# Kernel tuning notes

Hardware: AMD Instinct MI355X
Metric: run time of the kernel (lower is better)

## Reference

```python
import math
import jax, jax.numpy as jnp
import numpy as np

D = 512; H = 8; DH = 64          # d_model, heads, head dim
AB = 8                            # attention block size (BigBird block)
NG, NW, NR = 2, 5, 3              # global / window / random blocks
K = NG + NW + NR                  # attended blocks per query block
NL = 5                            # layers per (encoder|decoder) stack
MAXSEQ = 1024; BS = 4; NM = 4; LAT = 16; FF = 2048


def setup_inputs() -> dict:
    key = jax.random.key(0)
    ks = jax.random.split(key, 20)
    B = 32
    S_enc = MAXSEQ + 1
    nb_enc = (S_enc + AB - 1) // AB   # 129
    nb_dec = MAXSEQ // AB             # 128
    def n(i, shape, s=0.02):
        return jax.random.normal(ks[i], shape, jnp.float32) * s
    return {
        'x': jax.random.normal(ks[0], (B, MAXSEQ, BS * NM), jnp.float32),
        'eps': jax.random.normal(ks[1], (B, LAT), jnp.float32),
        'emb_in': n(2, (S_enc, D)),
        'emb_out': n(3, (MAXSEQ, D)),
        'W_data': n(4, (BS * NM, D)), 'b_data': jnp.zeros((D,), jnp.float32),
        'Wqkv': n(5, (2 * NL, D, 3 * D)), 'bqkv': jnp.zeros((2 * NL, 3 * D), jnp.float32),
        'Wo': n(6, (2 * NL, D, D)), 'bo': jnp.zeros((2 * NL, D), jnp.float32),
        'ln1_g': jnp.ones((2 * NL, D), jnp.float32), 'ln1_b': jnp.zeros((2 * NL, D), jnp.float32),
        'W1': n(7, (2 * NL, D, FF)), 'b1': jnp.zeros((2 * NL, FF), jnp.float32),
        'W2': n(8, (2 * NL, FF, D)), 'b2': jnp.zeros((2 * NL, D), jnp.float32),
        'ln2_g': jnp.ones((2 * NL, D), jnp.float32), 'ln2_b': jnp.zeros((2 * NL, D), jnp.float32),
        'W_mean': n(9, (D, LAT)), 'b_mean': jnp.zeros((LAT,), jnp.float32),
        'W_lv': n(10, (D, LAT)), 'b_lv': jnp.zeros((LAT,), jnp.float32),
        'W_exp': n(11, (LAT, 2 * MAXSEQ)), 'b_exp': jnp.zeros((2 * MAXSEQ,), jnp.float32),
        'W_conv': n(12, (2, D)), 'b_conv': jnp.zeros((D,), jnp.float32),
        'W_seq': n(13, (D, BS * NM)), 'b_seq': jnp.zeros((BS * NM,), jnp.float32),
        'rand_enc': jax.random.randint(ks[14], (nb_enc, NR), 0, nb_enc, jnp.int32),
        'rand_dec': jax.random.randint(ks[15], (nb_dec, NR), 0, nb_dec, jnp.int32),
    }


def _ln(x, g, b):
    m = jnp.mean(x, -1, keepdims=True)
    v = jnp.var(x, -1, keepdims=True)
    return (x - m) * jax.lax.rsqrt(v + 1e-5) * g + b


def _block_index(nb, rand):
    # per query block: NG global blocks, NW window blocks, NR random blocks
    i = jnp.arange(nb)
    g = jnp.broadcast_to(jnp.arange(NG)[None, :], (nb, NG))
    w = i[:, None] + (jnp.arange(NW) - NW // 2)[None, :]
    w_valid = (w >= 0) & (w < nb)
    idx = jnp.concatenate([g, jnp.clip(w, 0, nb - 1), rand], axis=1)          # [nb, K]
    valid = jnp.concatenate([jnp.ones((nb, NG), bool), w_valid,
                             jnp.ones((nb, NR), bool)], axis=1)               # [nb, K]
    return idx, valid


def _sparse_attn(x, Wqkv, bqkv, Wo, bo, rand):
    # BigBird-style block-sparse self attention (global + window + random blocks)
    B, S, _ = x.shape
    nb = (S + AB - 1) // AB
    Sp = nb * AB
    qkv = jnp.pad(x @ Wqkv + bqkv, ((0, 0), (0, Sp - S), (0, 0)))
    q, k, v = jnp.split(qkv, 3, axis=-1)
    def blk(t):  # [B,Sp,D] -> [B,H,nb,AB,DH]
        return t.reshape(B, nb, AB, H, DH).transpose(0, 3, 1, 2, 4)
    q, k, v = blk(q), blk(k), blk(v)
    idx, bvalid = _block_index(nb, rand)
    kg = k[:, :, idx]                      # [B,H,nb,K,AB,DH]
    vg = v[:, :, idx]
    scores = jnp.einsum('bhnqd,bhnkpd->bhnqkp', q, kg) / math.sqrt(DH)  # [B,H,nb,AB,K,AB]
    tok_valid = (jnp.arange(Sp) < S).reshape(nb, AB)
    kmask = bvalid[:, :, None] & tok_valid[idx]                          # [nb,K,AB]
    scores = jnp.where(kmask[None, None, :, None], scores, -1e9)
    attn = jax.nn.softmax(scores.reshape(B, H, nb, AB, K * AB), axis=-1)
    out = jnp.einsum('bhnqk,bhnkd->bhnqd', attn, vg.reshape(B, H, nb, K * AB, DH))
    out = out.transpose(0, 2, 3, 1, 4).reshape(B, Sp, D)[:, :S]
    return out @ Wo + bo


def _layer(x, i, p, rand):
    (Wqkv, bqkv, Wo, bo, ln1_g, ln1_b, W1, b1, W2, b2, ln2_g, ln2_b) = p
    a = _sparse_attn(x, Wqkv[i], bqkv[i], Wo[i], bo[i], rand)
    x = _ln(x + a, ln1_g[i], ln1_b[i])
    f = jax.nn.relu(x @ W1[i] + b1[i]) @ W2[i] + b2[i]
    return _ln(x + f, ln2_g[i], ln2_b[i])


def _forward(x, eps, emb_in, emb_out, W_data, b_data, Wqkv, bqkv, Wo, bo,
             ln1_g, ln1_b, W1, b1, W2, b2, ln2_g, ln2_b, W_mean, b_mean,
             W_lv, b_lv, W_exp, b_exp, W_conv, b_conv, W_seq, b_seq,
             rand_enc, rand_dec):
    B = x.shape[0]
    p = (Wqkv, bqkv, Wo, bo, ln1_g, ln1_b, W1, b1, W2, b2, ln2_g, ln2_b)
    # ---- encode ----
    h = x @ W_data + b_data                                   # [B,1024,512]
    cls = jnp.zeros((B, 1, D), x.dtype)
    h = jnp.concatenate([cls, h], axis=1) + emb_in            # [B,1025,512]
    for i in range(NL):
        h = _layer(h, i, p, rand_enc)
    pooled = h[:, 0]
    mean = pooled @ W_mean + b_mean
    logvar = pooled @ W_lv + b_lv
    # ---- sample (diag-Gaussian rsample) ----
    z = mean + eps * jnp.exp(0.5 * logvar)
    # ---- decode ----
    seq = (z @ W_exp + b_exp).reshape(B, 2, MAXSEQ)           # [B,2,1024]
    d = jnp.einsum('bcs,cd->bsd', seq, W_conv) + b_conv       # 1x1 conv, -> [B,1024,512]
    d = d + emb_out
    for i in range(NL, 2 * NL):
        d = _layer(d, i, p, rand_dec)
    out = d @ W_seq + b_seq                                   # [B,1024,16] (1x1 conv)
    decoded = out.reshape(B, -1, NM)                          # [B,4096,4]
    elbo = jnp.mean(-0.5 * jnp.sum(1.0 + logvar - mean ** 2 - jnp.exp(logvar), axis=1))
    return decoded, elbo


def reference(x, eps, emb_in, emb_out, W_data, b_data, Wqkv, bqkv, Wo, bo,
              ln1_g, ln1_b, W1, b1, W2, b2, ln2_g, ln2_b, W_mean, b_mean,
              W_lv, b_lv, W_exp, b_exp, W_conv, b_conv, W_seq, b_seq,
              rand_enc, rand_dec):
    return _forward(x, eps, emb_in, emb_out, W_data, b_data, Wqkv, bqkv, Wo, bo,
                    ln1_g, ln1_b, W1, b1, W2, b2, ln2_g, ln2_b, W_mean, b_mean,
                    W_lv, b_lv, W_exp, b_exp, W_conv, b_conv, W_seq, b_seq,
                    rand_enc, rand_dec)
```

## Files before the change

### kernel.cpp

```cpp
#include <hip/hip_runtime.h>

typedef unsigned short u16;
typedef __attribute__((ext_vector_type(8))) short short8;
typedef __attribute__((ext_vector_type(4))) float f32x4;

__device__ __forceinline__ float b2f(u16 h) {
  union { unsigned int u; float f; } v; v.u = ((unsigned int)h) << 16; return v.f;
}
__device__ __forceinline__ u16 f2b(float f) {
  union { float f; unsigned int u; } v; v.f = f;
  return (u16)((v.u + 0x7fffu + ((v.u >> 16) & 1u)) >> 16);
}

__device__ __forceinline__ void gload16(const u16* g, u16* l) {
  __builtin_amdgcn_global_load_lds(
      (const __attribute__((address_space(1))) void*)g,
      (__attribute__((address_space(3))) void*)l, 16, 0, 0);
}

#define SENC 1025
#define SPENC 1032
#define NBE 129
#define SDEC 1024
#define NBD 128
#define BATCH 32
#define MENC (BATCH * SPENC)
#define MDEC (BATCH * SDEC)

__global__ void beacon_k(float* out) { if (threadIdx.x == 0) out[0] = 1000.0f; }

__global__ __launch_bounds__(256) void tr_k(const float* __restrict__ W, u16* __restrict__ WT, int K, int N)
{
  __shared__ float sm[32][33];
  int k0 = blockIdx.x * 32, n0 = blockIdx.y * 32;
  const float* Wz = W + (size_t)blockIdx.z * K * N;
  u16* WTz = WT + (size_t)blockIdx.z * K * N;
  int r = threadIdx.x >> 3, c0 = (threadIdx.x & 7) * 4;
  float4 v = *(const float4*)&Wz[(size_t)(k0 + r) * N + n0 + c0];
  sm[r][c0] = v.x; sm[r][c0 + 1] = v.y; sm[r][c0 + 2] = v.z; sm[r][c0 + 3] = v.w;
  __syncthreads();
  ushort4 u;
  u.x = f2b(sm[c0][r]); u.y = f2b(sm[c0 + 1][r]); u.z = f2b(sm[c0 + 2][r]); u.w = f2b(sm[c0 + 3][r]);
  *(ushort4*)&WTz[(size_t)(n0 + r) * K + k0 + c0] = u;
}

__global__ __launch_bounds__(256) void embed_k(const float* __restrict__ x, const float* __restrict__ Wd,
    const float* __restrict__ bd, const float* __restrict__ emb, float* __restrict__ h, u16* __restrict__ hb)
{
  size_t gid = (size_t)blockIdx.x * 256 + threadIdx.x;
  int dd = (int)(gid & 511);
  size_t rs = gid >> 9;
  int s = (int)(rs % SPENC);
  int b = (int)(rs / SPENC);
  float v;
  if (s == 0) {
    v = emb[dd];
  } else if (s < SENC) {
    float acc = bd[dd];
    const float* xr = x + ((size_t)b * 1024 + (s - 1)) * 16;
    #pragma unroll
    for (int j = 0; j < 16; ++j) acc += xr[j] * Wd[j * 512 + dd];
    v = acc + emb[(size_t)s * 512 + dd];
  } else {
    v = 0.f;
  }
  h[gid] = v;
  hb[gid] = f2b(v);
}

template<bool RELU>
__global__ __launch_bounds__(512) void mgemm_k(const u16* __restrict__ A, const u16* __restrict__ WT,
    const float* __restrict__ bias, u16* __restrict__ C,
    int M, int N, int Kc, int lda, int ldb)
{
  __shared__ __align__(16) u16 sA[3][128 * 32];
  __shared__ __align__(16) u16 sB[3][256 * 32];
  int t = threadIdx.x;

  int gx = gridDim.x;
  int nwg = gx * gridDim.y;
  int flat = blockIdx.y * gx + blockIdx.x;
  int q = nwg >> 3, rr = nwg & 7;
  int xcd = flat & 7, idx = flat >> 3;
  int swz = (xcd < rr ? xcd * (q + 1) : rr * (q + 1) + (xcd - rr) * q) + idx;
  int bx = swz % gx, by = swz / gx;

  int n0 = bx * 256, m0 = by * 128;
  int lane = t & 63, wave = t >> 6;
  int wm = (wave >> 2) * 64, wn = (wave & 3) * 64;
  int quad = lane >> 4, l15 = lane & 15;

  int rA = t >> 2, sc = t & 3;
  int cA = sc ^ ((rA >> 1) & 3);
  int raA = m0 + rA; raA = raA < M ? raA : M - 1;
  const u16* gA  = A  + (size_t)raA * lda + cA * 8;
  const u16* gB0 = WT + (size_t)(n0 + rA) * ldb + cA * 8;
  const u16* gB1 = WT + (size_t)(n0 + 128 + rA) * ldb + cA * 8;

  f32x4 acc[4][4];
  #pragma unroll
  for (int i = 0; i < 4; ++i)
    #pragma unroll
    for (int j = 0; j < 4; ++j) acc[i][j] = (f32x4){0.f, 0.f, 0.f, 0.f};

  const int nt = Kc >> 5;
  gload16(gA,      &sA[0][t * 8]);
  gload16(gB0,     &sB[0][t * 8]);
  gload16(gB1,     &sB[0][(512 + t) * 8]);
  gload16(gA + 32, &sA[1][t * 8]);
  gload16(gB0 + 32,&sB[1][t * 8]);
  gload16(gB1 + 32,&sB[1][(512 + t) * 8]);

  int cur = 0;
  for (int tt = 0; tt < nt; ++tt) {
    if (tt < nt - 1) {
      asm volatile("s_waitcnt vmcnt(3)" ::: "memory");
    } else {
      asm volatile("s_waitcnt vmcnt(0)" ::: "memory");
    }
    __builtin_amdgcn_s_barrier();
    asm volatile("" ::: "memory");
    if (tt + 2 < nt) {
      int k0 = (tt + 2) << 5;
      int nb = tt + 2; nb -= (nb / 3) * 3;
      gload16(gA + k0,  &sA[nb][t * 8]);
      gload16(gB0 + k0, &sB[nb][t * 8]);
      gload16(gB1 + k0, &sB[nb][(512 + t) * 8]);
    }
    short8 af[4], bf[4];
    #pragma unroll
    for (int i = 0; i < 4; ++i) {
      int ra = wm + i * 16 + l15;
      af[i] = *(const short8*)&sA[cur][ra * 32 + (quad ^ ((ra >> 1) & 3)) * 8];
    }
    #pragma unroll
    for (int j = 0; j < 4; ++j) {
      int rb = wn + j * 16 + l15;
      bf[j] = *(const short8*)&sB[cur][rb * 32 + (quad ^ ((rb >> 1) & 3)) * 8];
    }
    __builtin_amdgcn_s_setprio(1);
    #pragma unroll
    for (int i = 0; i < 4; ++i)
      #pragma unroll
      for (int j = 0; j < 4; ++j)
        acc[i][j] = __builtin_amdgcn_mfma_f32_16x16x32_bf16(af[i], bf[j], acc[i][j], 0, 0, 0);
    __builtin_amdgcn_s_setprio(0);
    cur = (cur == 2) ? 0 : cur + 1;
  }

  #pragma unroll
  for (int i = 0; i < 4; ++i) {
    int mBase = m0 + wm + i * 16 + quad * 4;
    #pragma unroll
    for (int r = 0; r < 4; ++r) {
      int m = mBase + r;
      if (m < M) {
        #pragma unroll
        for (int j = 0; j < 4; ++j) {
          int n = n0 + wn + j * 16 + l15;
          float v = acc[i][j][r] + bias[n];
          if (RELU) v = fmaxf(v, 0.f);
          C[(size_t)m * N + n] = f2b(v);
        }
      }
    }
  }
}

__global__ __launch_bounds__(512) void mgemmln_k(const u16* __restrict__ A, const u16* __restrict__ WT,
    const float* __restrict__ bias, float* __restrict__ h, u16* __restrict__ hb,
    const float* __restrict__ g, const float* __restrict__ bbv_,
    int M, int Kc, int lda)
{
  __shared__ __align__(16) u16 sA[2][128 * 32];
  __shared__ __align__(16) u16 sB[2][512 * 32];
  __shared__ float redS[128][4], redQ[128][4];
  int t = threadIdx.x;
  int m0 = blockIdx.x * 128;
  int lane = t & 63, wave = t >> 6;
  int wm = (wave >> 2) * 64, wn = (wave & 3) * 128;
  int quad = lane >> 4, l15 = lane & 15;
  int wnid = wave & 3;

  int rA = t >> 2, sc = t & 3;
  int cA = sc ^ ((rA >> 1) & 3);
  const u16* gA = A + (size_t)(m0 + rA) * lda + cA * 8;
  const u16* gB = WT + (size_t)rA * Kc + cA * 8;

  f32x4 acc[4][8];
  #pragma unroll
  for (int i = 0; i < 4; ++i)
    #pragma unroll
    for (int j = 0; j < 8; ++j) acc[i][j] = (f32x4){0.f, 0.f, 0.f, 0.f};

  const int nt = Kc >> 5;
  gload16(gA, &sA[0][t * 8]);
  #pragma unroll
  for (int b4 = 0; b4 < 4; ++b4)
    gload16(gB + (size_t)b4 * 128 * Kc, &sB[0][(b4 * 512 + t) * 8]);
  int cur = 0;
  for (int tt = 0; tt < nt; ++tt) {
    __syncthreads();
    if (tt + 1 < nt) {
      int k0 = (tt + 1) << 5;
      gload16(gA + k0, &sA[cur ^ 1][t * 8]);
      #pragma unroll
      for (int b4 = 0; b4 < 4; ++b4)
        gload16(gB + (size_t)b4 * 128 * Kc + k0, &sB[cur ^ 1][(b4 * 512 + t) * 8]);
    }
    short8 af[4], bf[8];
    #pragma unroll
    for (int i = 0; i < 4; ++i) {
      int ra = wm + i * 16 + l15;
      af[i] = *(const short8*)&sA[cur][ra * 32 + (quad ^ ((ra >> 1) & 3)) * 8];
    }
    #pragma unroll
    for (int j = 0; j < 8; ++j) {
      int rb = wn + j * 16 + l15;
      bf[j] = *(const short8*)&sB[cur][rb * 32 + (quad ^ ((rb >> 1) & 3)) * 8];
    }
    __builtin_amdgcn_s_setprio(1);
    #pragma unroll
    for (int i = 0; i < 4; ++i)
      #pragma unroll
      for (int j = 0; j < 8; ++j)
        acc[i][j] = __builtin_amdgcn_mfma_f32_16x16x32_bf16(af[i], bf[j], acc[i][j], 0, 0, 0);
    __builtin_amdgcn_s_setprio(0);
    cur ^= 1;
  }

  float bsv[8];
  #pragma unroll
  for (int j = 0; j < 8; ++j) bsv[j] = bias[wn + j * 16 + l15];

  #pragma unroll
  for (int i = 0; i < 4; ++i) {
    #pragma unroll
    for (int r = 0; r < 4; ++r) {
      int lr = wm + i * 16 + quad * 4 + r;
      const float* hrow = h + (size_t)(m0 + lr) * 512 + wn + l15;
      float s = 0.f, qq = 0.f;
      #pragma unroll
      for (int j = 0; j < 8; ++j) {
        float v = acc[i][j][r] + bsv[j] + hrow[j * 16];
        acc[i][j][r] = v;
        s += v; qq += v * v;
      }
      #pragma unroll
      for (int off = 1; off < 16; off <<= 1) {
        s += __shfl_xor(s, off);
        qq += __shfl_xor(qq, off);
      }
      if (l15 == 0) { redS[lr][wnid] = s; redQ[lr][wnid] = qq; }
    }
  }
  __syncthreads();
  float gv[8], bv[8];
  #pragma unroll
  for (int j = 0; j < 8; ++j) {
    gv[j] = g[wn + j * 16 + l15];
    bv[j] = bbv_[wn + j * 16 + l15];
  }
  #pragma unroll
  for (int i = 0; i < 4; ++i) {
    #pragma unroll
    for (int r = 0; r < 4; ++r) {
      int lr = wm + i * 16 + quad * 4 + r;
      float s = redS[lr][0] + redS[lr][1] + redS[lr][2] + redS[lr][3];
      float qq = redQ[lr][0] + redQ[lr][1] + redQ[lr][2] + redQ[lr][3];
      float mean = s * (1.f / 512.f);
      float var = fmaxf(qq * (1.f / 512.f) - mean * mean, 0.f);
      float rinv = rsqrtf(var + 1e-5f);
      float* hrow = h + (size_t)(m0 + lr) * 512 + wn + l15;
      u16* hbrow = hb + (size_t)(m0 + lr) * 512 + wn + l15;
      #pragma unroll
      for (int j = 0; j < 8; ++j) {
        float o = (acc[i][j][r] - mean) * rinv * gv[j] + bv[j];
        hrow[j * 16] = o;
        hbrow[j * 16] = f2b(o);
      }
    }
  }
}

__global__ __launch_bounds__(64) void attnm_k(const u16* __restrict__ qkv, u16* __restrict__ av,
    const int* __restrict__ rnd, int S, int Sp, int nb)
{
  __shared__ __align__(16) u16 Vt[64 * 104];
  __shared__ __align__(16) u16 Pl[16 * 104];
  __shared__ int sJB[10], sVD[10];
  int t = threadIdx.x;
  int n = blockIdx.x % nb;
  int r1 = blockIdx.x / nb;
  int hh = r1 & 7, b = r1 >> 3;
  const u16* base = qkv + (size_t)b * Sp * 1536;
  int l15 = t & 15, quad = t >> 4;

  if (t < 10) {
    int jb, vd;
    if (t < 2) { jb = t; vd = 1; }
    else if (t < 7) {
      int w = n + t - 4;
      vd = (w >= 0 && w < nb) ? 1 : 0;
      jb = w < 0 ? 0 : (w > nb - 1 ? nb - 1 : w);
    } else { jb = rnd[n * 3 + t - 7]; vd = 1; }
    sJB[t] = jb; sVD[t] = vd;
  }
  {
    f32x4 zz = {0.f, 0.f, 0.f, 0.f};
    *(f32x4*)&Vt[t * 104 + 80] = zz;
    *(f32x4*)&Vt[t * 104 + 88] = zz;
    if (t < 16) {
      *(f32x4*)&Pl[t * 104 + 80] = zz;
      *(f32x4*)&Pl[t * 104 + 88] = zz;
    }
  }
  __syncthreads();

  short8 aq0, aq1;
  {
    const u16* qp = base + (size_t)(n * 8 + (l15 & 7)) * 1536 + hh * 64 + quad * 8;
    aq0 = *(const short8*)qp;
    aq1 = *(const short8*)(qp + 32);
  }

  f32x4 s[5];
  float okm[5];
  #pragma unroll
  for (int tile = 0; tile < 5; ++tile) {
    int kb = tile * 2 + (l15 >> 3);
    int tok = sJB[kb] * 8 + (l15 & 7);
    okm[tile] = (sVD[kb] && tok < S) ? 0.f : -3.0e38f;
    const u16* kp = base + (size_t)tok * 1536 + 512 + hh * 64 + quad * 8;
    short8 k0 = *(const short8*)kp;
    short8 k1 = *(const short8*)(kp + 32);
    f32x4 c = {0.f, 0.f, 0.f, 0.f};
    c = __builtin_amdgcn_mfma_f32_16x16x32_bf16(aq0, k0, c, 0, 0, 0);
    c = __builtin_amdgcn_mfma_f32_16x16x32_bf16(aq1, k1, c, 0, 0, 0);
    s[tile] = c;
  }

  u16 vreg[80];
  #pragma unroll
  for (int vt = 0; vt < 10; ++vt) {
    const u16* vp = base + (size_t)(sJB[vt] * 8) * 1536 + 1024 + hh * 64 + t;
    #pragma unroll
    for (int j = 0; j < 8; ++j) vreg[vt * 8 + j] = vp[(size_t)j * 1536];
  }

  f32x4 mx = {-3.0e38f, -3.0e38f, -3.0e38f, -3.0e38f};
  #pragma unroll
  for (int tile = 0; tile < 5; ++tile) {
    #pragma unroll
    for (int r = 0; r < 4; ++r) {
      float v = s[tile][r] * 0.125f + okm[tile];
      s[tile][r] = v;
      mx[r] = fmaxf(mx[r], v);
    }
  }
  #pragma unroll
  for (int off = 1; off < 16; off <<= 1) {
    #pragma unroll
    for (int r = 0; r < 4; ++r) mx[r] = fmaxf(mx[r], __shfl_xor(mx[r], off));
  }
  f32x4 sm = {0.f, 0.f, 0.f, 0.f};
  #pragma unroll
  for (int tile = 0; tile < 5; ++tile) {
    #pragma unroll
    for (int r = 0; r < 4; ++r) {
      float e = __expf(s[tile][r] - mx[r]);
      s[tile][r] = e;
      sm[r] += e;
    }
  }
  #pragma unroll
  for (int off = 1; off < 16; off <<= 1) {
    #pragma unroll
    for (int r = 0; r < 4; ++r) sm[r] += __shfl_xor(sm[r], off);
  }

  #pragma unroll
  for (int tile = 0; tile < 5; ++tile)
    #pragma unroll
    for (int r = 0; r < 4; ++r)
      Pl[(quad * 4 + r) * 104 + tile * 16 + l15] = f2b(s[tile][r]);

  #pragma unroll
  for (int vt = 0; vt < 10; ++vt) {
    short8 w;
    #pragma unroll
    for (int j = 0; j < 8; ++j) ((u16*)&w)[j] = (short)vreg[vt * 8 + j];
    *(short8*)&Vt[t * 104 + vt * 8] = w;
  }
  __syncthreads();

  f32x4 o[4];
  #pragma unroll
  for (int dn = 0; dn < 4; ++dn) o[dn] = (f32x4){0.f, 0.f, 0.f, 0.f};
  #pragma unroll
  for (int ks = 0; ks < 3; ++ks) {
    short8 ap = *(const short8*)&Pl[l15 * 104 + ks * 32 + quad * 8];
    #pragma unroll
    for (int dn = 0; dn < 4; ++dn) {
      short8 bv = *(const short8*)&Vt[(dn * 16 + l15) * 104 + ks * 32 + quad * 8];
      o[dn] = __builtin_amdgcn_mfma_f32_16x16x32_bf16(ap, bv, o[dn], 0, 0, 0);
    }
  }

  if (quad < 2) {
    #pragma unroll
    for (int r = 0; r < 4; ++r) {
      int qi = quad * 4 + r;
      float inv = 1.f / sm[r];
      u16* op = av + ((size_t)b * Sp + n * 8 + qi) * 512 + hh * 64 + l15;
      #pragma unroll
      for (int dn = 0; dn < 4; ++dn)
        op[dn * 16] = f2b(o[dn][r] * inv);
    }
  }
}

__global__ __launch_bounds__(512) void head_k(const float* __restrict__ h,
    const float* __restrict__ Wm, const float* __restrict__ bm,
    const float* __restrict__ Wlv, const float* __restrict__ blv,
    const float* __restrict__ eps, float* __restrict__ z, float* out_elbo)
{
  __shared__ float red[512];
  int t = threadIdx.x;
  int b = t >> 4, i = t & 15;
  const float* p = h + (size_t)b * SPENC * 512;
  float am = bm[i], al = blv[i];
  for (int c = 0; c < 512; ++c) {
    float pv = p[c];
    am += pv * Wm[c * 16 + i];
    al += pv * Wlv[c * 16 + i];
  }
  z[t] = am + eps[t] * expf(0.5f * al);
  red[t] = -0.5f * (1.f + al - am * am - expf(al));
  __syncthreads();
  for (int o = 256; o > 0; o >>= 1) { if (t < o) red[t] += red[t + o]; __syncthreads(); }
  if (t == 0) out_elbo[0] = red[0] * (1.f / 32.f);
}

__global__ __launch_bounds__(256) void seq_k(const float* __restrict__ z, const float* __restrict__ We,
    const float* __restrict__ be, float* __restrict__ seq)
{
  int gid = blockIdx.x * 256 + threadIdx.x;
  int b = gid >> 11, c = gid & 2047;
  float acc = be[c];
  #pragma unroll
  for (int i = 0; i < 16; ++i) acc += z[b * 16 + i] * We[i * 2048 + c];
  seq[gid] = acc;
}

__global__ __launch_bounds__(256) void decinit_k(const float* __restrict__ seq, const float* __restrict__ Wc,
    const float* __restrict__ bc, const float* __restrict__ emb, float* __restrict__ h, u16* __restrict__ hb)
{
  size_t gid = (size_t)blockIdx.x * 256 + threadIdx.x;
  int dd = (int)(gid & 511);
  size_t rs = gid >> 9;
  int s = (int)(rs & 1023);
  int b = (int)(rs >> 10);
  float v = seq[b * 2048 + s] * Wc[dd] + seq[b * 2048 + 1024 + s] * Wc[512 + dd]
          + bc[dd] + emb[(size_t)s * 512 + dd];
  h[gid] = v;
  hb[gid] = f2b(v);
}

__global__ __launch_bounds__(256) void finalm_k(const u16* __restrict__ hb, const float* __restrict__ Ws,
    const float* __restrict__ bs, float* __restrict__ out)
{
  __shared__ __align__(16) u16 Wt[16 * 520];
  int t = threadIdx.x;
  for (int e = t; e < 8192; e += 256) {
    int k = e >> 4, n = e & 15;
    Wt[n * 520 + k] = f2b(Ws[e]);
  }
  __syncthreads();
  int lane = t & 63, wave = t >> 6;
  int quad = lane >> 4, l15 = lane & 15;
  int m0 = blockIdx.x * 64 + wave * 16;
  const u16* arow = hb + (size_t)(m0 + l15) * 512 + quad * 8;
  f32x4 acc = (f32x4){0.f, 0.f, 0.f, 0.f};
  #pragma unroll
  for (int ks = 0; ks < 16; ++ks) {
    short8 af = *(const short8*)(arow + ks * 32);
    short8 bf = *(const short8*)&Wt[l15 * 520 + ks * 32 + quad * 8];
    acc = __builtin_amdgcn_mfma_f32_16x16x32_bf16(af, bf, acc, 0, 0, 0);
  }
  #pragma unroll
  for (int r = 0; r < 4; ++r)
    out[(size_t)(m0 + quad * 4 + r) * 16 + l15] = acc[r] + bs[l15];
}

extern "C" void kernel_launch(void* const* d_in, const int* in_sizes, int n_in,
                              void* d_out, int out_size, void* d_ws, size_t ws_size,
                              hipStream_t stream) {
  float* out = (float*)d_out;
  (void)out_size; (void)ws_size;

  static const int EXP_DICT[30] = {
    524288, 512, 524800, 524288, 8192, 512, 7864320, 15360, 2621440, 5120,
    5120, 5120, 10485760, 20480, 10485760, 5120, 5120, 5120, 8192, 16,
    8192, 16, 32768, 2048, 1024, 512, 8192, 16, 387, 384 };
  bool dict_ok = (n_in == 30);
  if (dict_ok) for (int i = 0; i < 30; ++i) if (in_sizes[i] != EXP_DICT[i]) { dict_ok = false; break; }
  if (!dict_ok) { beacon_k<<<1, 64, 0, stream>>>(out); return; }

  const float* x      = (const float*)d_in[0];
  const float* eps    = (const float*)d_in[1];
  const float* emb_in = (const float*)d_in[2];
  const float* emb_out= (const float*)d_in[3];
  const float* W_data = (const float*)d_in[4];
  const float* b_data = (const float*)d_in[5];
  const float* Wqkv   = (const float*)d_in[6];
  const float* bqkv   = (const float*)d_in[7];
  const float* Wo     = (const float*)d_in[8];
  const float* bo     = (const float*)d_in[9];
  const float* ln1g   = (const float*)d_in[10];
  const float* ln1b   = (const float*)d_in[11];
  const float* W1     = (const float*)d_in[12];
  const float* b1     = (const float*)d_in[13];
  const float* W2     = (const float*)d_in[14];
  const float* b2     = (const float*)d_in[15];
  const float* ln2g   = (const float*)d_in[16];
  const float* ln2b   = (const float*)d_in[17];
  const float* Wm     = (const float*)d_in[18];
  const float* bm     = (const float*)d_in[19];
  const float* Wlv    = (const float*)d_in[20];
  const float* blv    = (const float*)d_in[21];
  const float* Wexp   = (const float*)d_in[22];
  const float* bexp   = (const float*)d_in[23];
  const float* Wconv  = (const float*)d_in[24];
  const float* bconv  = (const float*)d_in[25];
  const float* Wseq   = (const float*)d_in[26];
  const float* bseq   = (const float*)d_in[27];
  const int* rand_enc = (const int*)d_in[28];
  const int* rand_dec = (const int*)d_in[29];

  char* ws = (char*)d_ws;
  float* h     = (float*)ws;
  u16*   hb    = (u16*)(ws + 67633152);
  u16*   WTqkv = (u16*)(ws + 101449728);
  u16*   WTo   = (u16*)(ws + 117178368);
  u16*   WT1l  = (u16*)(ws + 122421248);
  u16*   WT2l  = (u16*)(ws + 124518400);
  u16*   qkvb  = (u16*)(ws + 126615552);
  u16*   avb   = (u16*)(ws + 126615552 + 50724864);
  u16*   ffnb  = (u16*)(ws + 126615552);
  float* seqb  = (float*)(ws + 194248704);
  float* z     = (float*)(ws + 194510848);

  tr_k<<<dim3(512 / 32, 1536 / 32, 10), 256, 0, stream>>>(Wqkv, WTqkv, 512, 1536);
  tr_k<<<dim3(512 / 32, 512 / 32, 10), 256, 0, stream>>>(Wo, WTo, 512, 512);

  {
    const int M = MENC;
    embed_k<<<(M * 512) / 256, 256, 0, stream>>>(x, W_data, b_data, emb_in, h, hb);
    for (int i = 0; i < 5; ++i) {
      for (int bc = 0; bc < 2; ++bc) {
        size_t roff = (size_t)bc * 16 * SPENC * 512;
        const int Mc = 16 * SPENC;
        const int ty = 129;
        mgemm_k<false><<<dim3(6, ty), 512, 0, stream>>>(
            hb + roff, WTqkv + (size_t)i * 512 * 1536, bqkv + (size_t)i * 1536, qkvb, Mc, 1536, 512, 512, 512);
        attnm_k<<<16 * 8 * NBE, 64, 0, stream>>>(qkvb, avb, rand_enc, SENC, SPENC, NBE);
        mgemmln_k<<<ty, 512, 0, stream>>>(
            avb, WTo + (size_t)i * 512 * 512, bo + (size_t)i * 512,
            h + roff, hb + roff, ln1g + (size_t)i * 512, ln1b + (size_t)i * 512, Mc, 512, 512);
      }
      tr_k<<<dim3(512 / 32, 2048 / 32, 1), 256, 0, stream>>>(W1 + (size_t)i * 512 * 2048, WT1l, 512, 2048);
      tr_k<<<dim3(2048 / 32, 512 / 32, 1), 256, 0, stream>>>(W2 + (size_t)i * 2048 * 512, WT2l, 2048, 512);
      for (int cc = 0; cc < 2; ++cc) {
        size_t off = (size_t)cc * 16512;
        const int Mc = 16512;
        const int ty = 129;
        mgemm_k<true><<<dim3(8, ty), 512, 0, stream>>>(
            hb + off * 512, WT1l, b1 + (size_t)i * 2048, ffnb, Mc, 2048, 512, 512, 512);
        mgemmln_k<<<ty, 512, 0, stream>>>(
            ffnb, WT2l, b2 + (size_t)i * 512,
            h + off * 512, hb + off * 512, ln2g + (size_t)i * 512, ln2b + (size_t)i * 512, Mc, 2048, 2048);
      }
    }
  }

  head_k<<<1, 512, 0, stream>>>(h, Wm, bm, Wlv, blv, eps, z, out + 524288);
  seq_k<<<256, 256, 0, stream>>>(z, Wexp, bexp, seqb);
  decinit_k<<<(MDEC * 512) / 256, 256, 0, stream>>>(seqb, Wconv, bconv, emb_out, h, hb);

  {
    for (int i = 5; i < 10; ++i) {
      for (int bc = 0; bc < 2; ++bc) {
        size_t roff = (size_t)bc * 16 * SDEC * 512;
        const int Mc = 16 * SDEC;
        const int ty = 128;
        mgemm_k<false><<<dim3(6, ty), 512, 0, stream>>>(
            hb + roff, WTqkv + (size_t)i * 512 * 1536, bqkv + (size_t)i * 1536, qkvb, Mc, 1536, 512, 512, 512);
        attnm_k<<<16 * 8 * NBD, 64, 0, stream>>>(qkvb, avb, rand_dec, SDEC, SDEC, NBD);
        mgemmln_k<<<ty, 512, 0, stream>>>(
            avb, WTo + (size_t)i * 512 * 512, bo + (size_t)i * 512,
            h + roff, hb + roff, ln1g + (size_t)i * 512, ln1b + (size_t)i * 512, Mc, 512, 512);
      }
      tr_k<<<dim3(512 / 32, 2048 / 32, 1), 256, 0, stream>>>(W1 + (size_t)i * 512 * 2048, WT1l, 512, 2048);
      tr_k<<<dim3(2048 / 32, 512 / 32, 1), 256, 0, stream>>>(W2 + (size_t)i * 2048 * 512, WT2l, 2048, 512);
      for (int cc = 0; cc < 2; ++cc) {
        size_t off = (size_t)cc * 16384;
        const int Mc = 16384;
        const int ty = 128;
        mgemm_k<true><<<dim3(8, ty), 512, 0, stream>>>(
            hb + off * 512, WT1l, b1 + (size_t)i * 2048, ffnb, Mc, 2048, 512, 512, 512);
        mgemmln_k<<<ty, 512, 0, stream>>>(
            ffnb, WT2l, b2 + (size_t)i * 512,
            h + off * 512, hb + off * 512, ln2g + (size_t)i * 512, ln2b + (size_t)i * 512, Mc, 2048, 2048);
      }
    }
  }

  finalm_k<<<MDEC / 64, 256, 0, stream>>>(hb, Wseq, bseq, out);
}
```

Measured before the change: 5.843 ms.

## Load GEMM operand fragments directly from global memory instead of staging through LDS

```diff
diff --git a/kernel.cpp b/kernel.cpp
--- a/kernel.cpp
+++ b/kernel.cpp
@@ -10,12 +10,6 @@
 __device__ __forceinline__ u16 f2b(float f) {
   union { float f; unsigned int u; } v; v.f = f;
   return (u16)((v.u + 0x7fffu + ((v.u >> 16) & 1u)) >> 16);
-}
-
-__device__ __forceinline__ void gload16(const u16* g, u16* l) {
-  __builtin_amdgcn_global_load_lds(
-      (const __attribute__((address_space(1))) void*)g,
-      (__attribute__((address_space(3))) void*)l, 16, 0, 0);
 }
 
 #define SENC 1025
@@ -73,8 +67,6 @@
     const float* __restrict__ bias, u16* __restrict__ C,
     int M, int N, int Kc, int lda, int ldb)
 {
-  __shared__ __align__(16) u16 sA[3][128 * 32];
-  __shared__ __align__(16) u16 sB[3][256 * 32];
   int t = threadIdx.x;
 
   int gx = gridDim.x;
@@ -90,12 +82,8 @@
   int wm = (wave >> 2) * 64, wn = (wave & 3) * 64;
   int quad = lane >> 4, l15 = lane & 15;
 
-  int rA = t >> 2, sc = t & 3;
-  int cA = sc ^ ((rA >> 1) & 3);
-  int raA = m0 + rA; raA = raA < M ? raA : M - 1;
-  const u16* gA  = A  + (size_t)raA * lda + cA * 8;
-  const u16* gB0 = WT + (size_t)(n0 + rA) * ldb + cA * 8;
-  const u16* gB1 = WT + (size_t)(n0 + 128 + rA) * ldb + cA * 8;
+  const u16* aB = A  + (size_t)(m0 + wm + l15) * lda + quad * 8;
+  const u16* bB = WT + (size_t)(n0 + wn + l15) * ldb + quad * 8;
 
   f32x4 acc[4][4];
   #pragma unroll
@@ -104,48 +92,35 @@
     for (int j = 0; j < 4; ++j) acc[i][j] = (f32x4){0.f, 0.f, 0.f, 0.f};
 
   const int nt = Kc >> 5;
-  gload16(gA,      &sA[0][t * 8]);
-  gload16(gB0,     &sB[0][t * 8]);
-  gload16(gB1,     &sB[0][(512 + t) * 8]);
-  gload16(gA + 32, &sA[1][t * 8]);
-  gload16(gB0 + 32,&sB[1][t * 8]);
-  gload16(gB1 + 32,&sB[1][(512 + t) * 8]);
-
-  int cur = 0;
-  for (int tt = 0; tt < nt; ++tt) {
-    if (tt < nt - 1) {
-      asm volatile("s_waitcnt vmcnt(3)" ::: "memory");
-    } else {
-      asm volatile("s_waitcnt vmcnt(0)" ::: "memory");
-    }
-    __builtin_amdgcn_s_barrier();
-    asm volatile("" ::: "memory");
-    if (tt + 2 < nt) {
-      int k0 = (tt + 2) << 5;
-      int nb = tt + 2; nb -= (nb / 3) * 3;
-      gload16(gA + k0,  &sA[nb][t * 8]);
-      gload16(gB0 + k0, &sB[nb][t * 8]);
-      gload16(gB1 + k0, &sB[nb][(512 + t) * 8]);
-    }
-    short8 af[4], bf[4];
-    #pragma unroll
-    for (int i = 0; i < 4; ++i) {
-      int ra = wm + i * 16 + l15;
-      af[i] = *(const short8*)&sA[cur][ra * 32 + (quad ^ ((ra >> 1) & 3)) * 8];
-    }
-    #pragma unroll
-    for (int j = 0; j < 4; ++j) {
-      int rb = wn + j * 16 + l15;
-      bf[j] = *(const short8*)&sB[cur][rb * 32 + (quad ^ ((rb >> 1) & 3)) * 8];
-    }
-    __builtin_amdgcn_s_setprio(1);
+  short8 afA[4], bfA[4], afB[4], bfB[4];
+  #pragma unroll
+  for (int i = 0; i < 4; ++i) afA[i] = *(const short8*)(aB + (size_t)i * 16 * lda);
+  #pragma unroll
+  for (int j = 0; j < 4; ++j) bfA[j] = *(const short8*)(bB + (size_t)j * 16 * ldb);
+
+  for (int kk = 0; kk < nt; kk += 2) {
+    int ko1 = (kk + 1) << 5;
+    #pragma unroll
+    for (int i = 0; i < 4; ++i) afB[i] = *(const short8*)(aB + (size_t)i * 16 * lda + ko1);
+    #pragma unroll
+    for (int j = 0; j < 4; ++j) bfB[j] = *(const short8*)(bB + (size_t)j * 16 * ldb + ko1);
     #pragma unroll
     for (int i = 0; i < 4; ++i)
       #pragma unroll
       for (int j = 0; j < 4; ++j)
-        acc[i][j] = __builtin_amdgcn_mfma_f32_16x16x32_bf16(af[i], bf[j], acc[i][j], 0, 0, 0);
-    __builtin_amdgcn_s_setprio(0);
-    cur = (cur == 2) ? 0 : cur + 1;
+        acc[i][j] = __builtin_amdgcn_mfma_f32_16x16x32_bf16(afA[i], bfA[j], acc[i][j], 0, 0, 0);
+    if (kk + 2 < nt) {
+      int ko2 = (kk + 2) << 5;
+      #pragma unroll
+      for (int i = 0; i < 4; ++i) afA[i] = *(const short8*)(aB + (size_t)i * 16 * lda + ko2);
+      #pragma unroll
+      for (int j = 0; j < 4; ++j) bfA[j] = *(const short8*)(bB + (size_t)j * 16 * ldb + ko2);
+    }
+    #pragma unroll
+    for (int i = 0; i < 4; ++i)
+      #pragma unroll
+      for (int j = 0; j < 4; ++j)
+        acc[i][j] = __builtin_amdgcn_mfma_f32_16x16x32_bf16(afB[i], bfB[j], acc[i][j], 0, 0, 0);
   }
 
   #pragma unroll
@@ -172,8 +147,6 @@
     const float* __restrict__ g, const float* __restrict__ bbv_,
     int M, int Kc, int lda)
 {
-  __shared__ __align__(16) u16 sA[2][128 * 32];
-  __shared__ __align__(16) u16 sB[2][512 * 32];
   __shared__ float redS[128][4], redQ[128][4];
   int t = threadIdx.x;
   int m0 = blockIdx.x * 128;
@@ -182,10 +155,8 @@
   int quad = lane >> 4, l15 = lane & 15;
   int wnid = wave & 3;
 
-  int rA = t >> 2, sc = t & 3;
-  int cA = sc ^ ((rA >> 1) & 3);
-  const u16* gA = A + (size_t)(m0 + rA) * lda + cA * 8;
-  const u16* gB = WT + (size_t)rA * Kc + cA * 8;
+  const u16* aB = A  + (size_t)(m0 + wm + l15) * lda + quad * 8;
+  const u16* bB = WT + (size_t)(wn + l15) * Kc + quad * 8;
 
   f32x4 acc[4][8];
   #pragma unroll
@@ -194,39 +165,18 @@
     for (int j = 0; j < 8; ++j) acc[i][j] = (f32x4){0.f, 0.f, 0.f, 0.f};
 
   const int nt = Kc >> 5;
-  gload16(gA, &sA[0][t * 8]);
-  #pragma unroll
-  for (int b4 = 0; b4 < 4; ++b4)
-    gload16(gB + (size_t)b4 * 128 * Kc, &sB[0][(b4 * 512 + t) * 8]);
-  int cur = 0;
-  for (int tt = 0; tt < nt; ++tt) {
-    __syncthreads();
-    if (tt + 1 < nt) {
-      int k0 = (tt + 1) << 5;
-      gload16(gA + k0, &sA[cur ^ 1][t * 8]);
-      #pragma unroll
-      for (int b4 = 0; b4 < 4; ++b4)
-        gload16(gB + (size_t)b4 * 128 * Kc + k0, &sB[cur ^ 1][(b4 * 512 + t) * 8]);
-    }
+  for (int kk = 0; kk < nt; ++kk) {
+    int ko = kk << 5;
     short8 af[4], bf[8];
     #pragma unroll
-    for (int i = 0; i < 4; ++i) {
-      int ra = wm + i * 16 + l15;
-      af[i] = *(const short8*)&sA[cur][ra * 32 + (quad ^ ((ra >> 1) & 3)) * 8];
-    }
-    #pragma unroll
-    for (int j = 0; j < 8; ++j) {
-      int rb = wn + j * 16 + l15;
-      bf[j] = *(const short8*)&sB[cur][rb * 32 + (quad ^ ((rb >> 1) & 3)) * 8];
-    }
-    __builtin_amdgcn_s_setprio(1);
+    for (int i = 0; i < 4; ++i) af[i] = *(const short8*)(aB + (size_t)i * 16 * lda + ko);
+    #pragma unroll
+    for (int j = 0; j < 8; ++j) bf[j] = *(const short8*)(bB + (size_t)j * 16 * Kc + ko);
     #pragma unroll
     for (int i = 0; i < 4; ++i)
       #pragma unroll
       for (int j = 0; j < 8; ++j)
         acc[i][j] = __builtin_amdgcn_mfma_f32_16x16x32_bf16(af[i], bf[j], acc[i][j], 0, 0, 0);
-    __builtin_amdgcn_s_setprio(0);
-    cur ^= 1;
   }
 
   float bsv[8];
```

Measured after the change: 11.51 ms. +96.9%, slower.
